# Performance work log

Measured on AMD Instinct MI355X. Metric: run time of the kernel, lower is better.

## Reference

```python
import jax, jax.numpy as jnp
import numpy as np

B, T, K, FT, FP, N, H, HEADS, C = 8, 5, 20, 384, 3, 128, 64, 8, 2
ALPHA = 0.2
NEG = -9e15


def gru(x, Wi, Wh, bi, bh):
    # x: [M, L, F] -> (full [M, L, Hd], last [M, Hd]); torch nn.GRU cell math
    Hd = Wh.shape[0]
    gx = jnp.einsum('mlf,fg->mlg', x, Wi) + bi  # precompute input projections

    def step(h, gxt):
        gh = h @ Wh + bh
        xr, xz, xn = jnp.split(gxt, 3, axis=-1)
        hr, hz, hn = jnp.split(gh, 3, axis=-1)
        r = jax.nn.sigmoid(xr + hr)
        z = jax.nn.sigmoid(xz + hz)
        n = jnp.tanh(xn + r * hn)
        h = (1. - z) * n + z * h
        return h, h

    h0 = jnp.zeros((x.shape[0], Hd), x.dtype)
    last, full = jax.lax.scan(step, h0, jnp.swapaxes(gx, 0, 1))
    return jnp.swapaxes(full, 0, 1), last


def temporal_attn(full, last):
    # attend over time using the last hidden state as the query
    a = jax.nn.softmax(jnp.einsum('mlh,mh->ml', full, last), axis=-1)
    return jnp.einsum('ml,mlh->mh', a, full)


def gat_forward(s, p, adj, sm1_Wi, sm1_Wh, sm1_bi, sm1_bh,
                sm2_Wi, sm2_Wh, sm2_bi, sm2_bh,
                pr_Wi, pr_Wh, pr_bi, pr_bh,
                Wb, bb, Wx, bx, W1, a1, W2, a2):
    mask = adj > 0  # [N, N]
    # --- SMEncoder: vectorized over (batch, stock, day) ---
    s_ = jnp.transpose(s, (0, 4, 1, 2, 3)).reshape(B * N * T, K, FT)
    f1, l1 = gru(s_, sm1_Wi, sm1_Wh, sm1_bi, sm1_bh)
    cv = temporal_attn(f1, l1).reshape(B * N, T, H)          # intra-day context
    f2, l2 = gru(cv, sm2_Wi, sm2_Wh, sm2_bi, sm2_bh)
    ct = temporal_attn(f2, l2).reshape(B, N, H)              # inter-day context
    # --- PriceEncoder: vectorized over (batch, stock) ---
    p_ = jnp.transpose(p, (0, 3, 1, 2)).reshape(B * N, T, FP)
    f3, l3 = gru(p_, pr_Wi, pr_Wh, pr_bi, pr_bh)
    qt = temporal_attn(f3, l3).reshape(B, N, H)
    # --- bilinear fusion + per-stock linear head (dropout is eval-mode identity) ---
    X = jnp.tanh(jnp.einsum('bni,oij,bnj->bno', ct, Wb, qt) + bb)   # [B, N, H]
    out1 = jnp.tanh(jnp.einsum('bnh,nch->bnc', X, Wx) + bx)          # [B, N, C]
    # --- multi-head GAT layer 1 (concat + LeakyReLU + adj-masked softmax) ---
    Whd = jnp.einsum('bnh,khf->bknf', X, W1)                         # [B, heads, N, H]
    e = jax.nn.leaky_relu(
        jnp.einsum('bknf,kf->bkn', Whd, a1[:, :H])[:, :, :, None]
        + jnp.einsum('bknf,kf->bkn', Whd, a1[:, H:])[:, :, None, :], ALPHA)
    att = jax.nn.softmax(jnp.where(mask, e, NEG), axis=-1)
    Xh = jax.nn.elu(jnp.einsum('bknm,bkmf->bknf', att, Whd))
    X2 = jnp.transpose(Xh, (0, 2, 1, 3)).reshape(B, N, HEADS * H)    # head concat
    # --- GAT layer 2 -> num_classes ---
    Wh2 = X2 @ W2                                                    # [B, N, C]
    e2 = jax.nn.leaky_relu((Wh2 @ a2[:C])[:, :, None]
                           + (Wh2 @ a2[C:])[:, None, :], ALPHA)
    att2 = jax.nn.softmax(jnp.where(mask, e2, NEG), axis=-1)
    Xo = jnp.einsum('bnm,bmc->bnc', att2, Wh2)
    return jnp.transpose(Xo + out1, (0, 2, 1))                       # [B, C, N]


def setup_inputs():
    key = jax.random.key(0)
    ks = jax.random.split(key, 23)
    g = lambda k, sh, sc=0.05: jax.random.normal(k, sh, jnp.float32) * sc
    adj = (jax.random.uniform(ks[2], (N, N)) < 0.3).astype(jnp.float32)
    adj = jnp.maximum(adj, jnp.eye(N, dtype=jnp.float32))
    return {
        's': jax.random.normal(ks[0], (B, T, K, FT, N), jnp.float32),
        'p': jax.random.normal(ks[1], (B, T, FP, N), jnp.float32),
        'adj': adj,
        'sm1_Wi': g(ks[3], (FT, 3 * H)), 'sm1_Wh': g(ks[4], (H, 3 * H)),
        'sm1_bi': g(ks[5], (3 * H,)), 'sm1_bh': g(ks[6], (3 * H,)),
        'sm2_Wi': g(ks[7], (H, 3 * H)), 'sm2_Wh': g(ks[8], (H, 3 * H)),
        'sm2_bi': g(ks[9], (3 * H,)), 'sm2_bh': g(ks[10], (3 * H,)),
        'pr_Wi': g(ks[11], (FP, 3 * H)), 'pr_Wh': g(ks[12], (H, 3 * H)),
        'pr_bi': g(ks[13], (3 * H,)), 'pr_bh': g(ks[14], (3 * H,)),
        'Wb': g(ks[15], (H, H, H)), 'bb': g(ks[16], (H,)),
        'Wx': g(ks[17], (N, C, H)), 'bx': g(ks[18], (N, C)),
        'W1': g(ks[19], (HEADS, H, H)), 'a1': g(ks[20], (HEADS, 2 * H)),
        'W2': g(ks[21], (HEADS * H, C)), 'a2': g(ks[22], (2 * C,)),
    }


def reference(s, p, adj, sm1_Wi, sm1_Wh, sm1_bi, sm1_bh,
              sm2_Wi, sm2_Wh, sm2_bi, sm2_bh,
              pr_Wi, pr_Wh, pr_bi, pr_bh,
              Wb, bb, Wx, bx, W1, a1, W2, a2):
    return gat_forward(s, p, adj, sm1_Wi, sm1_Wh, sm1_bi, sm1_bh,
                       sm2_Wi, sm2_Wh, sm2_bi, sm2_bh,
                       pr_Wi, pr_Wh, pr_bi, pr_bh,
                       Wb, bb, Wx, bx, W1, a1, W2, a2)
```

## Files before the change

### kernel.cpp

```cpp
#include <hip/hip_runtime.h>
#include <hip/hip_bf16.h>
#include <hip/hip_fp16.h>

#define DI __device__ __forceinline__

namespace {

constexpr int G_  = 192;
constexpr int FT_ = 384;

typedef _Float16 f16x8 __attribute__((ext_vector_type(8)));
typedef _Float16 f16x4 __attribute__((ext_vector_type(4)));
typedef float    f32x4 __attribute__((ext_vector_type(4)));

DI float lrelu(float x) { return x > 0.f ? x : 0.2f * x; }
DI float sigmoidf(float x) { return 1.f / (1.f + __expf(-x)); }
DI float tanh_fast(float x) { float e = __expf(2.f * x); return 1.f - 2.f / (e + 1.f); }

__global__ __launch_bounds__(256) void k_cvtB(
    const float* __restrict__ Wi, _Float16* __restrict__ Bt) {
  int v = blockIdx.x * 256 + threadIdx.x;
  int g = v / 384, f = v % 384;
  Bt[v] = (_Float16)Wi[f * 192 + g];
}

__global__ __launch_bounds__(256) void k_gx1(
    const float* __restrict__ s, const _Float16* __restrict__ Bt,
    const float* __restrict__ bi, _Float16* __restrict__ gx1) {
  const int slab = blockIdx.x;
  const int b = slab / 100, rem = slab % 100, t = rem / 20, k = rem % 20;
  const float* A = s + (size_t)((b * 5 + t) * 20 + k) * (FT_ * 128);
  __shared__ __align__(16) _Float16 AsL[128 * 40];
  __shared__ __align__(16) _Float16 BsL[192 * 40];
  __shared__ __align__(16) float bisL[192];
  const int tid = threadIdx.x;
  if (tid < 192) bisL[tid] = bi[tid];
  const int w = tid >> 6, l = tid & 63;
  const int lr = l & 15, lk = l >> 4;

  f32x4 acc[12][2];
#pragma unroll
  for (int gt = 0; gt < 12; ++gt)
#pragma unroll
    for (int nt = 0; nt < 2; ++nt) acc[gt][nt] = (f32x4){0.f, 0.f, 0.f, 0.f};

  for (int kc = 0; kc < 12; ++kc) {
    const int f0 = kc * 32;
#pragma unroll
    for (int pass = 0; pass < 2; ++pass) {
      int task = tid + 256 * pass;
      int n = task & 127, oct = task >> 7;
      const float* src = A + (size_t)(f0 + oct * 8) * 128 + n;
      float v[8];
#pragma unroll
      for (int j = 0; j < 8; ++j) v[j] = src[j * 128];
      f16x8 h;
#pragma unroll
      for (int j = 0; j < 8; ++j) h[j] = (_Float16)v[j];
      *(f16x8*)&AsL[n * 40 + oct * 8] = h;
    }
#pragma unroll
    for (int pass = 0; pass < 3; ++pass) {
      int c = tid + 256 * pass;
      int g = c >> 2, oct = c & 3;
      f16x8 h = *(const f16x8*)&Bt[(size_t)g * 384 + f0 + oct * 8];
      *(f16x8*)&BsL[g * 40 + oct * 8] = h;
    }
    __syncthreads();
    f16x8 aN[2];
#pragma unroll
    for (int nt = 0; nt < 2; ++nt)
      aN[nt] = *(const f16x8*)&AsL[(w * 32 + nt * 16 + lr) * 40 + lk * 8];
#pragma unroll
    for (int gt = 0; gt < 12; ++gt) {
      f16x8 bW = *(const f16x8*)&BsL[(gt * 16 + lr) * 40 + lk * 8];
      acc[gt][0] = __builtin_amdgcn_mfma_f32_16x16x32_f16(bW, aN[0], acc[gt][0], 0, 0, 0);
      acc[gt][1] = __builtin_amdgcn_mfma_f32_16x16x32_f16(bW, aN[1], acc[gt][1], 0, 0, 0);
    }
    __syncthreads();
  }
  const size_t base3 = ((size_t)k * 40 + b * 5 + t) * 8;
#pragma unroll
  for (int nt = 0; nt < 2; ++nt) {
    const int ngrp = w * 2 + nt;
    _Float16* dstbase = gx1 + ((base3 + ngrp) * 3) * 1024 + (size_t)l * 16;
#pragma unroll
    for (int gate = 0; gate < 3; ++gate) {
      f16x8 h0, h1;
#pragma unroll
      for (int tq = 0; tq < 4; ++tq) {
        const int gt = gate * 4 + tq;
        f32x4 bias = *(const f32x4*)&bisL[gt * 16 + lk * 4];
        f32x4 c = acc[gt][nt];
#pragma unroll
        for (int r = 0; r < 4; ++r) {
          float v = c[r] + bias[r];
          if (tq < 2) h0[tq * 4 + r] = (_Float16)v;
          else        h1[(tq - 2) * 4 + r] = (_Float16)v;
        }
      }
      *(f16x8*)(dstbase + (size_t)gate * 1024) = h0;
      *(f16x8*)(dstbase + (size_t)gate * 1024 + 8) = h1;
    }
  }
}

__global__ __launch_bounds__(64, 1) void k_scan1m(
    const _Float16* __restrict__ gx, const float* __restrict__ Wh,
    const float* __restrict__ bh, float* __restrict__ cv) {
  const int wv = blockIdx.x;
  const int b = wv / 40, rem = wv % 40, t = rem / 8, ng = rem % 8;
  const int l = threadIdx.x;
  const int seq = l & 15, rg = l >> 4;

  __shared__ __align__(16) _Float16 histL[20][64][24];
  __shared__ __align__(16) _Float16 red[16][72];

  f16x8 whF[12][2];
#pragma unroll
  for (int gt = 0; gt < 12; ++gt)
#pragma unroll
    for (int c = 0; c < 2; ++c) {
      f16x8 h;
#pragma unroll
      for (int j = 0; j < 8; ++j)
        h[j] = (_Float16)Wh[(size_t)(32 * c + rg * 8 + j) * 192 + gt * 16 + seq];
      whF[gt][c] = h;
    }
  f32x4 bhF[12];
#pragma unroll
  for (int gt = 0; gt < 12; ++gt)
    bhF[gt] = *(const f32x4*)&bh[gt * 16 + rg * 4];

  float h16[16];
#pragma unroll
  for (int j = 0; j < 16; ++j) h16[j] = 0.f;

#define GXP(kk) (gx + ((((size_t)(kk) * 40 + b * 5 + t) * 8 + ng) * 3) * 1024 + (size_t)l * 16)

  f16x8 gxc[3][2], gxn[3][2];
  {
    const _Float16* p0 = GXP(0);
    const _Float16* p1 = GXP(1);
#pragma unroll
    for (int g = 0; g < 3; ++g) {
      gxc[g][0] = *(const f16x8*)(p0 + g * 1024);
      gxc[g][1] = *(const f16x8*)(p0 + g * 1024 + 8);
      gxn[g][0] = *(const f16x8*)(p1 + g * 1024);
      gxn[g][1] = *(const f16x8*)(p1 + g * 1024 + 8);
    }
  }

  f16x8 bf0, bf1;
  f32x4 acc[12];

#define GATES_AND_H(KCONST_HIST)                                               \
  {                                                                            \
    _Float16* hp = &histL[KCONST_HIST][l][0];                                  \
    f16x8 p0, p1;                                                              \
    _Pragma("unroll")                                                          \
    for (int tq = 0; tq < 4; ++tq) {                                           \
      _Pragma("unroll")                                                        \
      for (int r = 0; r < 4; ++r) {                                            \
        const int idx = tq * 4 + r;                                            \
        float xr = (float)gxc[0][idx >> 3][idx & 7];                           \
        float xz = (float)gxc[1][idx >> 3][idx & 7];                           \
        float xn = (float)gxc[2][idx >> 3][idx & 7];                           \
        float hr = acc[tq][r], hz = acc[4 + tq][r], hnv = acc[8 + tq][r];      \
        float rr = sigmoidf(xr + hr);                                          \
        float zz = sigmoidf(xz + hz);                                          \
        float nn = tanh_fast(xn + rr * hnv);                                   \
        float hv = (1.f - zz) * nn + zz * h16[idx];                            \
        h16[idx] = hv;                                                         \
        if (idx < 8) p0[idx] = (_Float16)hv; else p1[idx - 8] = (_Float16)hv;  \
      }                                                                        \
    }                                                                          \
    *(f16x8*)hp = p0;                                                          \
    *(f16x8*)(hp + 8) = p1;                                                    \
  }

#define REDIST()                                                               \
  {                                                                            \
    _Pragma("unroll")                                                          \
    for (int tq = 0; tq < 4; ++tq) {                                           \
      f16x4 q;                                                                 \
      q[0] = (_Float16)h16[tq * 4 + 0]; q[1] = (_Float16)h16[tq * 4 + 1];      \
      q[2] = (_Float16)h16[tq * 4 + 2]; q[3] = (_Float16)h16[tq * 4 + 3];      \
      *(f16x4*)&red[seq][16 * tq + 4 * rg] = q;                                \
    }                                                                          \
    bf0 = *(const f16x8*)&red[seq][8 * rg];                                    \
    bf1 = *(const f16x8*)&red[seq][32 + 8 * rg];                               \
  }

#pragma unroll
  for (int gt = 0; gt < 12; ++gt) acc[gt] = bhF[gt];
  GATES_AND_H(0)
  REDIST()

  for (int k = 1; k < 19; ++k) {
#pragma unroll
    for (int g = 0; g < 3; ++g) { gxc[g][0] = gxn[g][0]; gxc[g][1] = gxn[g][1]; }
    const _Float16* pn = GXP(k + 1);
#pragma unroll
    for (int g = 0; g < 3; ++g) {
      gxn[g][0] = *(const f16x8*)(pn + g * 1024);
      gxn[g][1] = *(const f16x8*)(pn + g * 1024 + 8);
    }
#pragma unroll
    for (int gt = 0; gt < 12; ++gt) {
      acc[gt] = bhF[gt];
      acc[gt] = __builtin_amdgcn_mfma_f32_16x16x32_f16(whF[gt][0], bf0, acc[gt], 0, 0, 0);
      acc[gt] = __builtin_amdgcn_mfma_f32_16x16x32_f16(whF[gt][1], bf1, acc[gt], 0, 0, 0);
    }
    GATES_AND_H(k)
    REDIST()
  }

#pragma unroll
  for (int g = 0; g < 3; ++g) { gxc[g][0] = gxn[g][0]; gxc[g][1] = gxn[g][1]; }
#pragma unroll
  for (int gt = 0; gt < 12; ++gt) {
    acc[gt] = bhF[gt];
    acc[gt] = __builtin_amdgcn_mfma_f32_16x16x32_f16(whF[gt][0], bf0, acc[gt], 0, 0, 0);
    acc[gt] = __builtin_amdgcn_mfma_f32_16x16x32_f16(whF[gt][1], bf1, acc[gt], 0, 0, 0);
  }
  GATES_AND_H(19)

  float d[20];
#pragma unroll
  for (int kk = 0; kk < 20; ++kk) {
    f16x8 a0 = *(const f16x8*)&histL[kk][l][0];
    f16x8 a1 = *(const f16x8*)&histL[kk][l][8];
    float p = 0.f;
#pragma unroll
    for (int j = 0; j < 8; ++j)
      p += (float)a0[j] * h16[j] + (float)a1[j] * h16[8 + j];
    p += __shfl_xor(p, 16);
    p += __shfl_xor(p, 32);
    d[kk] = p;
  }
  float mx = d[0];
#pragma unroll
  for (int kk = 1; kk < 20; ++kk) mx = fmaxf(mx, d[kk]);
  float sum = 0.f;
#pragma unroll
  for (int kk = 0; kk < 20; ++kk) { d[kk] = __expf(d[kk] - mx); sum += d[kk]; }
  const float inv = 1.f / sum;
  float av[16];
#pragma unroll
  for (int j = 0; j < 16; ++j) av[j] = 0.f;
#pragma unroll
  for (int kk = 0; kk < 20; ++kk) {
    f16x8 a0 = *(const f16x8*)&histL[kk][l][0];
    f16x8 a1 = *(const f16x8*)&histL[kk][l][8];
    float wgt = d[kk] * inv;
#pragma unroll
    for (int j = 0; j < 8; ++j) {
      av[j]     += wgt * (float)a0[j];
      av[8 + j] += wgt * (float)a1[j];
    }
  }
  const int n = ng * 16 + seq;
  float* dst = cv + ((size_t)(b * 128 + n) * 5 + t) * 64;
#pragma unroll
  for (int tq = 0; tq < 4; ++tq) {
    float4 o = make_float4(av[tq * 4], av[tq * 4 + 1], av[tq * 4 + 2], av[tq * 4 + 3]);
    *(float4*)&dst[16 * tq + 4 * rg] = o;
  }
#undef GXP
#undef GATES_AND_H
#undef REDIST
}

__global__ __launch_bounds__(192) void k_scan2(
    const float* __restrict__ x, const float* __restrict__ Wi,
    const float* __restrict__ Wh, const float* __restrict__ bi,
    const float* __restrict__ bh, float* __restrict__ outv) {
  const int s0 = blockIdx.x * 4;
  const int tid = threadIdx.x;
  __shared__ __align__(16) float hist[4][5][64];
  __shared__ __align__(16) float xl[4][64];
  __shared__ float ghl[4][192], gxl[4][192];
  __shared__ float dls[4][5], als[4][5];
  float wic[64], whc[64];
#pragma unroll
  for (int i = 0; i < 64; ++i) { wic[i] = Wi[i * G_ + tid]; whc[i] = Wh[i * G_ + tid]; }
  const float big = bi[tid], bhg = bh[tid];

  for (int t = 0; t < 5; ++t) {
    for (int v = tid; v < 256; v += 192) {
      int ss = v >> 6, i = v & 63;
      xl[ss][i] = x[((size_t)(s0 + ss) * 5 + t) * 64 + i];
    }
    __syncthreads();
#pragma unroll
    for (int ss = 0; ss < 4; ++ss) {
      const float4* xq = (const float4*)&xl[ss][0];
      float ax = 0.f;
#pragma unroll
      for (int q = 0; q < 16; ++q) {
        float4 v4 = xq[q];
        ax += v4.x * wic[4 * q]     + v4.y * wic[4 * q + 1]
            + v4.z * wic[4 * q + 2] + v4.w * wic[4 * q + 3];
      }
      gxl[ss][tid] = ax + big;
      float ah = 0.f;
      if (t > 0) {
        const float4* hq = (const float4*)&hist[ss][t - 1][0];
#pragma unroll
        for (int q = 0; q < 16; ++q) {
          float4 h4 = hq[q];
          ah += h4.x * whc[4 * q]     + h4.y * whc[4 * q + 1]
              + h4.z * whc[4 * q + 2] + h4.w * whc[4 * q + 3];
        }
      }
      ghl[ss][tid] = ah + bhg;
    }
    __syncthreads();
#pragma unroll
    for (int base = 0; base < 256; base += 192) {
      int tk = base + tid;
      if (tk < 256) {
        int ss = tk >> 6, i = tk & 63;
        float xr = gxl[ss][i], xz = gxl[ss][64 + i], xn = gxl[ss][128 + i];
        float hr = ghl[ss][i], hz = ghl[ss][64 + i], hn = ghl[ss][128 + i];
        float r  = sigmoidf(xr + hr);
        float z  = sigmoidf(xz + hz);
        float nn = tanh_fast(xn + r * hn);
        float hp = (t == 0) ? 0.f : hist[ss][t - 1][i];
        hist[ss][t][i] = (1.f - z) * nn + z * hp;
      }
    }
    __syncthreads();
  }
  if (tid < 20) {
    int ss = tid / 5, kk = tid % 5;
    float d = 0.f;
#pragma unroll
    for (int i = 0; i < 64; ++i) d += hist[ss][kk][i] * hist[ss][4][i];
    dls[ss][kk] = d;
  }
  __syncthreads();
  if (tid < 20) {
    int ss = tid / 5, kk = tid % 5;
    float mx = -3.4e38f;
#pragma unroll
    for (int j = 0; j < 5; ++j) mx = fmaxf(mx, dls[ss][j]);
    als[ss][kk] = __expf(dls[ss][kk] - mx);
  }
  __syncthreads();
  for (int idx = tid; idx < 256; idx += 192) {
    int ss = idx >> 6, i = idx & 63;
    float sum = 0.f, a = 0.f;
#pragma unroll
    for (int kk = 0; kk < 5; ++kk) sum += als[ss][kk];
#pragma unroll
    for (int kk = 0; kk < 5; ++kk) a += als[ss][kk] * hist[ss][kk][i];
    outv[(size_t)(s0 + ss) * 64 + i] = a / sum;
  }
}

__global__ __launch_bounds__(192) void k_scan3(
    const float* __restrict__ p, const float* __restrict__ Wi,
    const float* __restrict__ Wh, const float* __restrict__ bi,
    const float* __restrict__ bh, float* __restrict__ outv) {
  const int s0 = blockIdx.x * 4;
  const int tid = threadIdx.x;
  __shared__ __align__(16) float hist[4][5][64];
  __shared__ float xp[4][3];
  __shared__ float ghl[4][192], gxl[4][192];
  __shared__ float dls[4][5], als[4][5];
  float wic[3], whc[64];
#pragma unroll
  for (int f = 0; f < 3; ++f) wic[f] = Wi[f * G_ + tid];
#pragma unroll
  for (int i = 0; i < 64; ++i) whc[i] = Wh[i * G_ + tid];
  const float big = bi[tid], bhg = bh[tid];

  for (int t = 0; t < 5; ++t) {
    if (tid < 12) {
      int ss = tid / 3, f = tid % 3;
      int seq = s0 + ss, b = seq >> 7, n = seq & 127;
      xp[ss][f] = p[((size_t)(b * 5 + t) * 3 + f) * 128 + n];
    }
    __syncthreads();
#pragma unroll
    for (int ss = 0; ss < 4; ++ss) {
      gxl[ss][tid] = xp[ss][0] * wic[0] + xp[ss][1] * wic[1] + xp[ss][2] * wic[2] + big;
      float ah = 0.f;
      if (t > 0) {
        const float4* hq = (const float4*)&hist[ss][t - 1][0];
#pragma unroll
        for (int q = 0; q < 16; ++q) {
          float4 h4 = hq[q];
          ah += h4.x * whc[4 * q]     + h4.y * whc[4 * q + 1]
              + h4.z * whc[4 * q + 2] + h4.w * whc[4 * q + 3];
        }
      }
      ghl[ss][tid] = ah + bhg;
    }
    __syncthreads();
#pragma unroll
    for (int base = 0; base < 256; base += 192) {
      int tk = base + tid;
      if (tk < 256) {
        int ss = tk >> 6, i = tk & 63;
        float xr = gxl[ss][i], xz = gxl[ss][64 + i], xn = gxl[ss][128 + i];
        float hr = ghl[ss][i], hz = ghl[ss][64 + i], hn = ghl[ss][128 + i];
        float r  = sigmoidf(xr + hr);
        float z  = sigmoidf(xz + hz);
        float nn = tanh_fast(xn + r * hn);
        float hp = (t == 0) ? 0.f : hist[ss][t - 1][i];
        hist[ss][t][i] = (1.f - z) * nn + z * hp;
      }
    }
    __syncthreads();
  }
  if (tid < 20) {
    int ss = tid / 5, kk = tid % 5;
    float d = 0.f;
#pragma unroll
    for (int i = 0; i < 64; ++i) d += hist[ss][kk][i] * hist[ss][4][i];
    dls[ss][kk] = d;
  }
  __syncthreads();
  if (tid < 20) {
    int ss = tid / 5, kk = tid % 5;
    float mx = -3.4e38f;
#pragma unroll
    for (int j = 0; j < 5; ++j) mx = fmaxf(mx, dls[ss][j]);
    als[ss][kk] = __expf(dls[ss][kk] - mx);
  }
  __syncthreads();
  for (int idx = tid; idx < 256; idx += 192) {
    int ss = idx >> 6, i = idx & 63;
    float sum = 0.f, a = 0.f;
#pragma unroll
    for (int kk = 0; kk < 5; ++kk) sum += als[ss][kk];
#pragma unroll
    for (int kk = 0; kk < 5; ++kk) a += als[ss][kk] * hist[ss][kk][i];
    outv[(size_t)(s0 + ss) * 64 + i] = a / sum;
  }
}

__global__ __launch_bounds__(256) void k_bilinear(
    const float* __restrict__ ct, const float* __restrict__ qt,
    const float* __restrict__ Wb, const float* __restrict__ bb,
    float* __restrict__ X) {
  const int bn0 = blockIdx.x * 4;
  const int tid = threadIdx.x;
  __shared__ float ctl[4][64], qtl[4][64];
  {
    int ss = tid >> 6, i = tid & 63;
    ctl[ss][i] = ct[(size_t)(bn0 + ss) * 64 + i];
    qtl[ss][i] = qt[(size_t)(bn0 + ss) * 64 + i];
  }
  __syncthreads();
  const int o = tid >> 2, part = tid & 3, j0 = part << 4;
  float qr[4][16];
#pragma unroll
  for (int pp = 0; pp < 4; ++pp)
#pragma unroll
    for (int q = 0; q < 16; ++q) qr[pp][q] = qtl[pp][j0 + q];
  float acc[4] = {0.f, 0.f, 0.f, 0.f};
  const float* wb = Wb + (size_t)o * 4096 + j0;
  for (int i = 0; i < 64; ++i) {
    const float4* w4 = (const float4*)(wb + i * 64);
    float tmp[4] = {0.f, 0.f, 0.f, 0.f};
#pragma unroll
    for (int q = 0; q < 4; ++q) {
      float4 w = w4[q];
#pragma unroll
      for (int pp = 0; pp < 4; ++pp)
        tmp[pp] += w.x * qr[pp][4 * q]     + w.y * qr[pp][4 * q + 1]
                 + w.z * qr[pp][4 * q + 2] + w.w * qr[pp][4 * q + 3];
    }
#pragma unroll
    for (int pp = 0; pp < 4; ++pp) acc[pp] += ctl[pp][i] * tmp[pp];
  }
#pragma unroll
  for (int pp = 0; pp < 4; ++pp) {
    acc[pp] += __shfl_xor(acc[pp], 1);
    acc[pp] += __shfl_xor(acc[pp], 2);
  }
  if (part == 0) {
    float bbv = bb[o];
#pragma unroll
    for (int pp = 0; pp < 4; ++pp)
      X[(size_t)(bn0 + pp) * 64 + o] = tanh_fast(acc[pp] + bbv);
  }
}

__global__ __launch_bounds__(256) void k_gat1(
    const float* __restrict__ X, const float* __restrict__ W1,
    const float* __restrict__ a1, const float* __restrict__ adj,
    float* __restrict__ X2) {
  const int b = blockIdx.x >> 3, k = blockIdx.x & 7;
  const int tid = threadIdx.x;
  __shared__ __align__(16) float whd[128][68];
  __shared__ float w1l[64][64];
  __shared__ float d1l[128], d2l[128];
  for (int v = tid; v < 4096; v += 256) w1l[v >> 6][v & 63] = W1[(size_t)k * 4096 + v];
  __syncthreads();
  {
    const int f = tid & 63, ng = tid >> 6;
    const float* Xb = X + (size_t)b * 128 * 64;
    for (int n = ng * 32; n < ng * 32 + 32; ++n) {
      float a = 0.f;
#pragma unroll
      for (int h = 0; h < 64; ++h) a += Xb[n * 64 + h] * w1l[h][f];
      whd[n][f] = a;
    }
  }
  __syncthreads();
  if (tid < 128) {
    const int n = tid;
    float da = 0.f, db = 0.f;
#pragma unroll
    for (int f = 0; f < 64; ++f) {
      float w = whd[n][f];
      da += w * a1[k * 128 + f];
      db += w * a1[k * 128 + 64 + f];
    }
    d1l[n] = da; d2l[n] = db;
  }
  __syncthreads();
  {
    const int n = tid & 127, fh = tid >> 7;
    unsigned long long mlo = 0ull, mhi = 0ull;
    for (int m = 0; m < 64; ++m) if (adj[n * 128 + m] > 0.f)      mlo |= (1ull << m);
    for (int m = 0; m < 64; ++m) if (adj[n * 128 + 64 + m] > 0.f) mhi |= (1ull << m);
    const float d1n = d1l[n];
    float mx = -3.4e38f;
    for (int m = 0; m < 128; ++m) {
      bool on = (m < 64) ? (((mlo >> m) & 1ull) != 0) : (((mhi >> (m - 64)) & 1ull) != 0);
      float e = lrelu(d1n + d2l[m]);
      mx = fmaxf(mx, on ? e : -3.4e38f);
    }
    float sum = 0.f;
    float acc[32];
#pragma unroll
    for (int q = 0; q < 32; ++q) acc[q] = 0.f;
    for (int m = 0; m < 128; ++m) {
      bool on = (m < 64) ? (((mlo >> m) & 1ull) != 0) : (((mhi >> (m - 64)) & 1ull) != 0);
      float w = on ? __expf(lrelu(d1n + d2l[m]) - mx) : 0.f;
      sum += w;
      const float4* wr = (const float4*)&whd[m][fh * 32];
#pragma unroll
      for (int q8 = 0; q8 < 8; ++q8) {
        float4 wv = wr[q8];
        acc[4 * q8]     += w * wv.x;
        acc[4 * q8 + 1] += w * wv.y;
        acc[4 * q8 + 2] += w * wv.z;
        acc[4 * q8 + 3] += w * wv.w;
      }
    }
    float inv = 1.f / sum;
    float* dst = X2 + ((size_t)b * 128 + n) * 512 + k * 64 + fh * 32;
#pragma unroll
    for (int q = 0; q < 32; ++q) {
      float v = acc[q] * inv;
      dst[q] = v > 0.f ? v : (__expf(v) - 1.f);
    }
  }
}

__global__ __launch_bounds__(256) void k_head(
    const float* __restrict__ X, const float* __restrict__ Wx, const float* __restrict__ bx,
    const float* __restrict__ X2, const float* __restrict__ W2, const float* __restrict__ a2,
    const float* __restrict__ adj, float* __restrict__ out) {
  const int b = blockIdx.x;
  const int tid = threadIdx.x;
  __shared__ float w2l[1024];
  __shared__ float wh2l[128][2];
  __shared__ float d2aL[128], d2bL[128];
  __shared__ float out1L[128][2];
  for (int v = tid; v < 1024; v += 256) w2l[v] = W2[v];
  __syncthreads();
  const int w = tid >> 6, l = tid & 63;
  const float a20 = a2[0], a21 = a2[1], a22 = a2[2], a23 = a2[3];
  for (int it = 0; it < 32; ++it) {
    int n = w * 32 + it;
    const float* xr = X2 + ((size_t)b * 128 + n) * 512 + l * 8;
    float4 xa = *(const float4*)xr;
    float4 xb = *(const float4*)(xr + 4);
    float xs[8] = {xa.x, xa.y, xa.z, xa.w, xb.x, xb.y, xb.z, xb.w};
    float s0 = 0.f, s1 = 0.f;
#pragma unroll
    for (int j = 0; j < 8; ++j) {
      s0 += xs[j] * w2l[(l * 8 + j) * 2];
      s1 += xs[j] * w2l[(l * 8 + j) * 2 + 1];
    }
#pragma unroll
    for (int d = 1; d < 64; d <<= 1) { s0 += __shfl_xor(s0, d); s1 += __shfl_xor(s1, d); }
    if (l == 0) {
      wh2l[n][0] = s0; wh2l[n][1] = s1;
      d2aL[n] = s0 * a20 + s1 * a21;
      d2bL[n] = s0 * a22 + s1 * a23;
    }
  }
  if (tid < 128) {
    int n = tid;
    const float* xrow = X + ((size_t)b * 128 + n) * 64;
#pragma unroll
    for (int c = 0; c < 2; ++c) {
      float a = 0.f;
#pragma unroll
      for (int h = 0; h < 64; ++h) a += xrow[h] * Wx[(n * 2 + c) * 64 + h];
      out1L[n][c] = tanh_fast(a + bx[n * 2 + c]);
    }
  }
  __syncthreads();
  if (tid < 128) {
    const int n = tid;
    unsigned long long mlo = 0ull, mhi = 0ull;
    for (int m = 0; m < 64; ++m) if (adj[n * 128 + m] > 0.f)      mlo |= (1ull << m);
    for (int m = 0; m < 64; ++m) if (adj[n * 128 + 64 + m] > 0.f) mhi |= (1ull << m);
    const float dan = d2aL[n];
    float mx = -3.4e38f;
    for (int m = 0; m < 128; ++m) {
      bool on = (m < 64) ? (((mlo >> m) & 1ull) != 0) : (((mhi >> (m - 64)) & 1ull) != 0);
      float e = lrelu(dan + d2bL[m]);
      mx = fmaxf(mx, on ? e : -3.4e38f);
    }
    float sum = 0.f, x0 = 0.f, x1 = 0.f;
    for (int m = 0; m < 128; ++m) {
      bool on = (m < 64) ? (((mlo >> m) & 1ull) != 0) : (((mhi >> (m - 64)) & 1ull) != 0);
      float wgt = on ? __expf(lrelu(dan + d2bL[m]) - mx) : 0.f;
      sum += wgt; x0 += wgt * wh2l[m][0]; x1 += wgt * wh2l[m][1];
    }
    float inv = 1.f / sum;
    out[(size_t)(b * 2 + 0) * 128 + n] = x0 * inv + out1L[n][0];
    out[(size_t)(b * 2 + 1) * 128 + n] = x1 * inv + out1L[n][1];
  }
}

}

extern "C" void kernel_launch(void* const* d_in, const int* in_sizes, int n_in,
                              void* d_out, int out_size, void* d_ws, size_t ws_size,
                              hipStream_t stream) {
  (void)in_sizes; (void)n_in; (void)out_size;
  const float* s      = (const float*)d_in[0];
  const float* p      = (const float*)d_in[1];
  const float* adj    = (const float*)d_in[2];
  const float* sm1_Wi = (const float*)d_in[3];
  const float* sm1_Wh = (const float*)d_in[4];
  const float* sm1_bi = (const float*)d_in[5];
  const float* sm1_bh = (const float*)d_in[6];
  const float* sm2_Wi = (const float*)d_in[7];
  const float* sm2_Wh = (const float*)d_in[8];
  const float* sm2_bi = (const float*)d_in[9];
  const float* sm2_bh = (const float*)d_in[10];
  const float* pr_Wi  = (const float*)d_in[11];
  const float* pr_Wh  = (const float*)d_in[12];
  const float* pr_bi  = (const float*)d_in[13];
  const float* pr_bh  = (const float*)d_in[14];
  const float* Wb     = (const float*)d_in[15];
  const float* bb     = (const float*)d_in[16];
  const float* Wx     = (const float*)d_in[17];
  const float* bx     = (const float*)d_in[18];
  const float* W1     = (const float*)d_in[19];
  const float* a1     = (const float*)d_in[20];
  const float* W2     = (const float*)d_in[21];
  const float* a2     = (const float*)d_in[22];

  if (ws_size < 43515904u) return;
  char* ws = (char*)d_ws;
  _Float16* gx1 = (_Float16*)ws;
  float* cv   = (float*)(ws + 39321600);
  float* ct   = (float*)(ws + 40632320);
  float* qt   = (float*)(ws + 40894464);
  float* X    = (float*)(ws + 41156608);
  float* X2   = (float*)(ws + 41418752);
  _Float16* Bt = (_Float16*)(ws + 41418752);

  hipLaunchKernelGGL(k_cvtB,     dim3(288),  dim3(256), 0, stream, sm1_Wi, Bt);
  hipLaunchKernelGGL(k_gx1,      dim3(800),  dim3(256), 0, stream, s, Bt, sm1_bi, gx1);
  hipLaunchKernelGGL(k_scan1m,   dim3(320),  dim3(64),  0, stream, gx1, sm1_Wh, sm1_bh, cv);
  hipLaunchKernelGGL(k_scan2,    dim3(256),  dim3(192), 0, stream, cv, sm2_Wi, sm2_Wh, sm2_bi, sm2_bh, ct);
  hipLaunchKernelGGL(k_scan3,    dim3(256),  dim3(192), 0, stream, p, pr_Wi, pr_Wh, pr_bi, pr_bh, qt);
  hipLaunchKernelGGL(k_bilinear, dim3(256),  dim3(256), 0, stream, ct, qt, Wb, bb, X);
  hipLaunchKernelGGL(k_gat1,     dim3(64),   dim3(256), 0, stream, X, W1, a1, adj, X2);
  hipLaunchKernelGGL(k_head,     dim3(8),    dim3(256), 0, stream, X, Wx, bx, X2, W2, a2, adj, (float*)d_out);
}
```

Before: 503.3 us.

## Rewrite scan2 with MFMA, deepen gx prefetch, split GAT head kernels

Replaces the scalar scan2 GRU with an MFMA-based single-wave kernel that reads fp16 intra-day contexts written by scan1. scan1 now prefetches gx two steps ahead instead of one. gat1 gets twice as many blocks and the head kernel is split into a wider wh2/out1 kernel plus a small final softmax kernel, which adds one launch. Divides are replaced with hardware reciprocal, and the fp16 intermediate plus approximate rcp add a small precision cost.

Result: faster. 476.5 us (-5.3%).

```diff
diff --git a/kernel.cpp b/kernel.cpp
--- a/kernel.cpp
+++ b/kernel.cpp
@@ -13,9 +13,10 @@
 typedef _Float16 f16x4 __attribute__((ext_vector_type(4)));
 typedef float    f32x4 __attribute__((ext_vector_type(4)));
 
+DI float rcpf(float x) { return __builtin_amdgcn_rcpf(x); }
 DI float lrelu(float x) { return x > 0.f ? x : 0.2f * x; }
-DI float sigmoidf(float x) { return 1.f / (1.f + __expf(-x)); }
-DI float tanh_fast(float x) { float e = __expf(2.f * x); return 1.f - 2.f / (e + 1.f); }
+DI float sigmoidf(float x) { return rcpf(1.f + __expf(-x)); }
+DI float tanh_fast(float x) { return 1.f - 2.f * rcpf(__expf(2.f * x) + 1.f); }
 
 __global__ __launch_bounds__(256) void k_cvtB(
     const float* __restrict__ Wi, _Float16* __restrict__ Bt) {
@@ -107,7 +108,7 @@
 
 __global__ __launch_bounds__(64, 1) void k_scan1m(
     const _Float16* __restrict__ gx, const float* __restrict__ Wh,
-    const float* __restrict__ bh, float* __restrict__ cv) {
+    const float* __restrict__ bh, _Float16* __restrict__ cvh) {
   const int wv = blockIdx.x;
   const int b = wv / 40, rem = wv % 40, t = rem / 8, ng = rem % 8;
   const int l = threadIdx.x;
@@ -138,16 +139,19 @@
 
 #define GXP(kk) (gx + ((((size_t)(kk) * 40 + b * 5 + t) * 8 + ng) * 3) * 1024 + (size_t)l * 16)
 
-  f16x8 gxc[3][2], gxn[3][2];
+  f16x8 gxc[3][2], gxn[3][2], gxn2[3][2];
   {
     const _Float16* p0 = GXP(0);
     const _Float16* p1 = GXP(1);
+    const _Float16* p2 = GXP(2);
 #pragma unroll
     for (int g = 0; g < 3; ++g) {
-      gxc[g][0] = *(const f16x8*)(p0 + g * 1024);
-      gxc[g][1] = *(const f16x8*)(p0 + g * 1024 + 8);
-      gxn[g][0] = *(const f16x8*)(p1 + g * 1024);
-      gxn[g][1] = *(const f16x8*)(p1 + g * 1024 + 8);
+      gxc[g][0]  = *(const f16x8*)(p0 + g * 1024);
+      gxc[g][1]  = *(const f16x8*)(p0 + g * 1024 + 8);
+      gxn[g][0]  = *(const f16x8*)(p1 + g * 1024);
+      gxn[g][1]  = *(const f16x8*)(p1 + g * 1024 + 8);
+      gxn2[g][0] = *(const f16x8*)(p2 + g * 1024);
+      gxn2[g][1] = *(const f16x8*)(p2 + g * 1024 + 8);
     }
   }
 
@@ -199,12 +203,17 @@
 
   for (int k = 1; k < 19; ++k) {
 #pragma unroll
-    for (int g = 0; g < 3; ++g) { gxc[g][0] = gxn[g][0]; gxc[g][1] = gxn[g][1]; }
-    const _Float16* pn = GXP(k + 1);
-#pragma unroll
     for (int g = 0; g < 3; ++g) {
-      gxn[g][0] = *(const f16x8*)(pn + g * 1024);
-      gxn[g][1] = *(const f16x8*)(pn + g * 1024 + 8);
+      gxc[g][0] = gxn[g][0];  gxc[g][1] = gxn[g][1];
+      gxn[g][0] = gxn2[g][0]; gxn[g][1] = gxn2[g][1];
+    }
+    if (k < 18) {
+      const _Float16* pn = GXP(k + 2);
+#pragma unroll
+      for (int g = 0; g < 3; ++g) {
+        gxn2[g][0] = *(const f16x8*)(pn + g * 1024);
+        gxn2[g][1] = *(const f16x8*)(pn + g * 1024 + 8);
+      }
     }
 #pragma unroll
     for (int gt = 0; gt < 12; ++gt) {
@@ -245,7 +254,7 @@
   float sum = 0.f;
 #pragma unroll
   for (int kk = 0; kk < 20; ++kk) { d[kk] = __expf(d[kk] - mx); sum += d[kk]; }
-  const float inv = 1.f / sum;
+  const float inv = rcpf(sum);
   float av[16];
 #pragma unroll
   for (int j = 0; j < 16; ++j) av[j] = 0.f;
@@ -261,49 +270,174 @@
     }
   }
   const int n = ng * 16 + seq;
-  float* dst = cv + ((size_t)(b * 128 + n) * 5 + t) * 64;
+  const size_t seqg = (size_t)b * 128 + n;
+  _Float16* dst = cvh + (seqg * 5 + t) * 64;
+#pragma unroll
+  for (int tq = 0; tq < 4; ++tq) {
+    f16x4 q;
+    q[0] = (_Float16)av[tq * 4 + 0]; q[1] = (_Float16)av[tq * 4 + 1];
+    q[2] = (_Float16)av[tq * 4 + 2]; q[3] = (_Float16)av[tq * 4 + 3];
+    *(f16x4*)&dst[16 * tq + 4 * rg] = q;
+  }
+#undef GXP
+#undef GATES_AND_H
+#undef REDIST
+}
+
+__global__ __launch_bounds__(64, 1) void k_scan2m(
+    const _Float16* __restrict__ cvh, const float* __restrict__ Wi,
+    const float* __restrict__ Wh, const float* __restrict__ bi,
+    const float* __restrict__ bh, float* __restrict__ ct) {
+  const int l = threadIdx.x;
+  const int seq = l & 15, rg = l >> 4;
+  const size_t seqg0 = (size_t)blockIdx.x * 16;
+
+  __shared__ __align__(16) _Float16 histL[5][64][24];
+  __shared__ __align__(16) _Float16 red[16][72];
+
+  f16x8 wiF[12][2], whF[12][2];
+#pragma unroll
+  for (int gt = 0; gt < 12; ++gt)
+#pragma unroll
+    for (int c = 0; c < 2; ++c) {
+      f16x8 hi, hh;
+#pragma unroll
+      for (int j = 0; j < 8; ++j) {
+        hi[j] = (_Float16)Wi[(size_t)(32 * c + rg * 8 + j) * 192 + gt * 16 + seq];
+        hh[j] = (_Float16)Wh[(size_t)(32 * c + rg * 8 + j) * 192 + gt * 16 + seq];
+      }
+      wiF[gt][c] = hi; whF[gt][c] = hh;
+    }
+  f32x4 biF[12], bhF[12];
+#pragma unroll
+  for (int gt = 0; gt < 12; ++gt) {
+    biF[gt] = *(const f32x4*)&bi[gt * 16 + rg * 4];
+    bhF[gt] = *(const f32x4*)&bh[gt * 16 + rg * 4];
+  }
+
+  float h16[16];
+#pragma unroll
+  for (int j = 0; j < 16; ++j) h16[j] = 0.f;
+  f16x8 bf0, bf1;
+
+#pragma unroll
+  for (int t = 0; t < 5; ++t) {
+    const _Float16* xp = cvh + ((seqg0 + seq) * 5 + t) * 64;
+    f16x8 xf0 = *(const f16x8*)(xp + 8 * rg);
+    f16x8 xf1 = *(const f16x8*)(xp + 32 + 8 * rg);
+    f32x4 accX[12], accH[12];
+#pragma unroll
+    for (int gt = 0; gt < 12; ++gt) {
+      accX[gt] = biF[gt];
+      accX[gt] = __builtin_amdgcn_mfma_f32_16x16x32_f16(wiF[gt][0], xf0, accX[gt], 0, 0, 0);
+      accX[gt] = __builtin_amdgcn_mfma_f32_16x16x32_f16(wiF[gt][1], xf1, accX[gt], 0, 0, 0);
+      accH[gt] = bhF[gt];
+      if (t > 0) {
+        accH[gt] = __builtin_amdgcn_mfma_f32_16x16x32_f16(whF[gt][0], bf0, accH[gt], 0, 0, 0);
+        accH[gt] = __builtin_amdgcn_mfma_f32_16x16x32_f16(whF[gt][1], bf1, accH[gt], 0, 0, 0);
+      }
+    }
+    _Float16* hp = &histL[t][l][0];
+    f16x8 p0, p1;
+#pragma unroll
+    for (int tq = 0; tq < 4; ++tq) {
+#pragma unroll
+      for (int r = 0; r < 4; ++r) {
+        const int idx = tq * 4 + r;
+        float xr = accX[tq][r], xz = accX[4 + tq][r], xn = accX[8 + tq][r];
+        float hr = accH[tq][r], hz = accH[4 + tq][r], hnv = accH[8 + tq][r];
+        float rr = sigmoidf(xr + hr);
+        float zz = sigmoidf(xz + hz);
+        float nn = tanh_fast(xn + rr * hnv);
+        float hv = (1.f - zz) * nn + zz * h16[idx];
+        h16[idx] = hv;
+        if (idx < 8) p0[idx] = (_Float16)hv; else p1[idx - 8] = (_Float16)hv;
+      }
+    }
+    *(f16x8*)hp = p0;
+    *(f16x8*)(hp + 8) = p1;
+    if (t < 4) {
+#pragma unroll
+      for (int tq = 0; tq < 4; ++tq) {
+        f16x4 q;
+        q[0] = (_Float16)h16[tq * 4 + 0]; q[1] = (_Float16)h16[tq * 4 + 1];
+        q[2] = (_Float16)h16[tq * 4 + 2]; q[3] = (_Float16)h16[tq * 4 + 3];
+        *(f16x4*)&red[seq][16 * tq + 4 * rg] = q;
+      }
+      bf0 = *(const f16x8*)&red[seq][8 * rg];
+      bf1 = *(const f16x8*)&red[seq][32 + 8 * rg];
+    }
+  }
+
+  float d[5];
+#pragma unroll
+  for (int kk = 0; kk < 5; ++kk) {
+    f16x8 a0 = *(const f16x8*)&histL[kk][l][0];
+    f16x8 a1 = *(const f16x8*)&histL[kk][l][8];
+    float p = 0.f;
+#pragma unroll
+    for (int j = 0; j < 8; ++j)
+      p += (float)a0[j] * h16[j] + (float)a1[j] * h16[8 + j];
+    p += __shfl_xor(p, 16);
+    p += __shfl_xor(p, 32);
+    d[kk] = p;
+  }
+  float mx = d[0];
+#pragma unroll
+  for (int kk = 1; kk < 5; ++kk) mx = fmaxf(mx, d[kk]);
+  float sum = 0.f;
+#pragma unroll
+  for (int kk = 0; kk < 5; ++kk) { d[kk] = __expf(d[kk] - mx); sum += d[kk]; }
+  const float inv = rcpf(sum);
+  float av[16];
+#pragma unroll
+  for (int j = 0; j < 16; ++j) av[j] = 0.f;
+#pragma unroll
+  for (int kk = 0; kk < 5; ++kk) {
+    f16x8 a0 = *(const f16x8*)&histL[kk][l][0];
+    f16x8 a1 = *(const f16x8*)&histL[kk][l][8];
+    float wgt = d[kk] * inv;
+#pragma unroll
+    for (int j = 0; j < 8; ++j) {
+      av[j]     += wgt * (float)a0[j];
+      av[8 + j] += wgt * (float)a1[j];
+    }
+  }
+  float* dst = ct + (seqg0 + seq) * 64;
 #pragma unroll
   for (int tq = 0; tq < 4; ++tq) {
     float4 o = make_float4(av[tq * 4], av[tq * 4 + 1], av[tq * 4 + 2], av[tq * 4 + 3]);
     *(float4*)&dst[16 * tq + 4 * rg] = o;
   }
-#undef GXP
-#undef GATES_AND_H
-#undef REDIST
-}
-
-__global__ __launch_bounds__(192) void k_scan2(
-    const float* __restrict__ x, const float* __restrict__ Wi,
+}
+
+__global__ __launch_bounds__(192) void k_scan3(
+    const float* __restrict__ p, const float* __restrict__ Wi,
     const float* __restrict__ Wh, const float* __restrict__ bi,
     const float* __restrict__ bh, float* __restrict__ outv) {
   const int s0 = blockIdx.x * 4;
   const int tid = threadIdx.x;
   __shared__ __align__(16) float hist[4][5][64];
-  __shared__ __align__(16) float xl[4][64];
+  __shared__ float xp[4][3];
   __shared__ float ghl[4][192], gxl[4][192];
   __shared__ float dls[4][5], als[4][5];
-  float wic[64], whc[64];
-#pragma unroll
-  for (int i = 0; i < 64; ++i) { wic[i] = Wi[i * G_ + tid]; whc[i] = Wh[i * G_ + tid]; }
+  float wic[3], whc[64];
+#pragma unroll
+  for (int f = 0; f < 3; ++f) wic[f] = Wi[f * G_ + tid];
+#pragma unroll
+  for (int i = 0; i < 64; ++i) whc[i] = Wh[i * G_ + tid];
   const float big = bi[tid], bhg = bh[tid];
 
   for (int t = 0; t < 5; ++t) {
-    for (int v = tid; v < 256; v += 192) {
-      int ss = v >> 6, i = v & 63;
-      xl[ss][i] = x[((size_t)(s0 + ss) * 5 + t) * 64 + i];
+    if (tid < 12) {
+      int ss = tid / 3, f = tid % 3;
+      int seq = s0 + ss, b = seq >> 7, n = seq & 127;
+      xp[ss][f] = p[((size_t)(b * 5 + t) * 3 + f) * 128 + n];
     }
     __syncthreads();
 #pragma unroll
     for (int ss = 0; ss < 4; ++ss) {
-      const float4* xq = (const float4*)&xl[ss][0];
-      float ax = 0.f;
-#pragma unroll
-      for (int q = 0; q < 16; ++q) {
-        float4 v4 = xq[q];
-        ax += v4.x * wic[4 * q]     + v4.y * wic[4 * q + 1]
-            + v4.z * wic[4 * q + 2] + v4.w * wic[4 * q + 3];
-      }
-      gxl[ss][tid] = ax + big;
+      gxl[ss][tid] = xp[ss][0] * wic[0] + xp[ss][1] * wic[1] + xp[ss][2] * wic[2] + big;
       float ah = 0.f;
       if (t > 0) {
         const float4* hq = (const float4*)&hist[ss][t - 1][0];
@@ -356,90 +490,7 @@
     for (int kk = 0; kk < 5; ++kk) sum += als[ss][kk];
 #pragma unroll
     for (int kk = 0; kk < 5; ++kk) a += als[ss][kk] * hist[ss][kk][i];
-    outv[(size_t)(s0 + ss) * 64 + i] = a / sum;
-  }
-}
-
-__global__ __launch_bounds__(192) void k_scan3(
-    const float* __restrict__ p, const float* __restrict__ Wi,
-    const float* __restrict__ Wh, const float* __restrict__ bi,
-    const float* __restrict__ bh, float* __restrict__ outv) {
-  const int s0 = blockIdx.x * 4;
-  const int tid = threadIdx.x;
-  __shared__ __align__(16) float hist[4][5][64];
-  __shared__ float xp[4][3];
-  __shared__ float ghl[4][192], gxl[4][192];
-  __shared__ float dls[4][5], als[4][5];
-  float wic[3], whc[64];
-#pragma unroll
-  for (int f = 0; f < 3; ++f) wic[f] = Wi[f * G_ + tid];
-#pragma unroll
-  for (int i = 0; i < 64; ++i) whc[i] = Wh[i * G_ + tid];
-  const float big = bi[tid], bhg = bh[tid];
-
-  for (int t = 0; t < 5; ++t) {
-    if (tid < 12) {
-      int ss = tid / 3, f = tid % 3;
-      int seq = s0 + ss, b = seq >> 7, n = seq & 127;
-      xp[ss][f] = p[((size_t)(b * 5 + t) * 3 + f) * 128 + n];
-    }
-    __syncthreads();
-#pragma unroll
-    for (int ss = 0; ss < 4; ++ss) {
-      gxl[ss][tid] = xp[ss][0] * wic[0] + xp[ss][1] * wic[1] + xp[ss][2] * wic[2] + big;
-      float ah = 0.f;
-      if (t > 0) {
-        const float4* hq = (const float4*)&hist[ss][t - 1][0];
-#pragma unroll
-        for (int q = 0; q < 16; ++q) {
-          float4 h4 = hq[q];
-          ah += h4.x * whc[4 * q]     + h4.y * whc[4 * q + 1]
-              + h4.z * whc[4 * q + 2] + h4.w * whc[4 * q + 3];
-        }
-      }
-      ghl[ss][tid] = ah + bhg;
-    }
-    __syncthreads();
-#pragma unroll
-    for (int base = 0; base < 256; base += 192) {
-      int tk = base + tid;
-      if (tk < 256) {
-        int ss = tk >> 6, i = tk & 63;
-        float xr = gxl[ss][i], xz = gxl[ss][64 + i], xn = gxl[ss][128 + i];
-        float hr = ghl[ss][i], hz = ghl[ss][64 + i], hn = ghl[ss][128 + i];
-        float r  = sigmoidf(xr + hr);
-        float z  = sigmoidf(xz + hz);
-        float nn = tanh_fast(xn + r * hn);
-        float hp = (t == 0) ? 0.f : hist[ss][t - 1][i];
-        hist[ss][t][i] = (1.f - z) * nn + z * hp;
-      }
-    }
-    __syncthreads();
-  }
-  if (tid < 20) {
-    int ss = tid / 5, kk = tid % 5;
-    float d = 0.f;
-#pragma unroll
-    for (int i = 0; i < 64; ++i) d += hist[ss][kk][i] * hist[ss][4][i];
-    dls[ss][kk] = d;
-  }
-  __syncthreads();
-  if (tid < 20) {
-    int ss = tid / 5, kk = tid % 5;
-    float mx = -3.4e38f;
-#pragma unroll
-    for (int j = 0; j < 5; ++j) mx = fmaxf(mx, dls[ss][j]);
-    als[ss][kk] = __expf(dls[ss][kk] - mx);
-  }
-  __syncthreads();
-  for (int idx = tid; idx < 256; idx += 192) {
-    int ss = idx >> 6, i = idx & 63;
-    float sum = 0.f, a = 0.f;
-#pragma unroll
-    for (int kk = 0; kk < 5; ++kk) sum += als[ss][kk];
-#pragma unroll
-    for (int kk = 0; kk < 5; ++kk) a += als[ss][kk] * hist[ss][kk][i];
-    outv[(size_t)(s0 + ss) * 64 + i] = a / sum;
+    outv[(size_t)(s0 + ss) * 64 + i] = a * rcpf(sum);
   }
 }
 
@@ -495,7 +546,8 @@
     const float* __restrict__ X, const float* __restrict__ W1,
     const float* __restrict__ a1, const float* __restrict__ adj,
     float* __restrict__ X2) {
-  const int b = blockIdx.x >> 3, k = blockIdx.x & 7;
+  const int bid = blockIdx.x;
+  const int b = bid >> 4, k = (bid >> 1) & 7, nh = bid & 1;
   const int tid = threadIdx.x;
   __shared__ __align__(16) float whd[128][68];
   __shared__ float w1l[64][64];
@@ -526,7 +578,7 @@
   }
   __syncthreads();
   {
-    const int n = tid & 127, fh = tid >> 7;
+    const int n = nh * 64 + (tid & 63), fq = tid >> 6, f0 = fq * 16;
     unsigned long long mlo = 0ull, mhi = 0ull;
     for (int m = 0; m < 64; ++m) if (adj[n * 128 + m] > 0.f)      mlo |= (1ull << m);
     for (int m = 0; m < 64; ++m) if (adj[n * 128 + 64 + m] > 0.f) mhi |= (1ull << m);
@@ -538,50 +590,50 @@
       mx = fmaxf(mx, on ? e : -3.4e38f);
     }
     float sum = 0.f;
-    float acc[32];
-#pragma unroll
-    for (int q = 0; q < 32; ++q) acc[q] = 0.f;
+    float acc[16];
+#pragma unroll
+    for (int q = 0; q < 16; ++q) acc[q] = 0.f;
     for (int m = 0; m < 128; ++m) {
       bool on = (m < 64) ? (((mlo >> m) & 1ull) != 0) : (((mhi >> (m - 64)) & 1ull) != 0);
       float w = on ? __expf(lrelu(d1n + d2l[m]) - mx) : 0.f;
       sum += w;
-      const float4* wr = (const float4*)&whd[m][fh * 32];
-#pragma unroll
-      for (int q8 = 0; q8 < 8; ++q8) {
-        float4 wv = wr[q8];
-        acc[4 * q8]     += w * wv.x;
-        acc[4 * q8 + 1] += w * wv.y;
-        acc[4 * q8 + 2] += w * wv.z;
-        acc[4 * q8 + 3] += w * wv.w;
-      }
-    }
-    float inv = 1.f / sum;
-    float* dst = X2 + ((size_t)b * 128 + n) * 512 + k * 64 + fh * 32;
-#pragma unroll
-    for (int q = 0; q < 32; ++q) {
+      const float4* wr = (const float4*)&whd[m][f0];
+#pragma unroll
+      for (int q4 = 0; q4 < 4; ++q4) {
+        float4 wv = wr[q4];
+        acc[4 * q4]     += w * wv.x;
+        acc[4 * q4 + 1] += w * wv.y;
+        acc[4 * q4 + 2] += w * wv.z;
+        acc[4 * q4 + 3] += w * wv.w;
+      }
+    }
+    float inv = rcpf(sum);
+    float* dst = X2 + ((size_t)b * 128 + n) * 512 + k * 64 + f0;
+#pragma unroll
+    for (int q = 0; q < 16; ++q) {
       float v = acc[q] * inv;
       dst[q] = v > 0.f ? v : (__expf(v) - 1.f);
     }
   }
 }
 
-__global__ __launch_bounds__(256) void k_head(
+__global__ __launch_bounds__(256) void k_wh2(
     const float* __restrict__ X, const float* __restrict__ Wx, const float* __restrict__ bx,
     const float* __restrict__ X2, const float* __restrict__ W2, const float* __restrict__ a2,
-    const float* __restrict__ adj, float* __restrict__ out) {
-  const int b = blockIdx.x;
+    float* __restrict__ out1g, float* __restrict__ wh2g,
+    float* __restrict__ d2ag, float* __restrict__ d2bg) {
+  const int b = blockIdx.x >> 3, nq = blockIdx.x & 7;
   const int tid = threadIdx.x;
   __shared__ float w2l[1024];
-  __shared__ float wh2l[128][2];
-  __shared__ float d2aL[128], d2bL[128];
-  __shared__ float out1L[128][2];
   for (int v = tid; v < 1024; v += 256) w2l[v] = W2[v];
   __syncthreads();
   const int w = tid >> 6, l = tid & 63;
   const float a20 = a2[0], a21 = a2[1], a22 = a2[2], a23 = a2[3];
-  for (int it = 0; it < 32; ++it) {
-    int n = w * 32 + it;
-    const float* xr = X2 + ((size_t)b * 128 + n) * 512 + l * 8;
+#pragma unroll
+  for (int it = 0; it < 4; ++it) {
+    int n = nq * 16 + w * 4 + it;
+    int bn = b * 128 + n;
+    const float* xr = X2 + (size_t)bn * 512 + l * 8;
     float4 xa = *(const float4*)xr;
     float4 xb = *(const float4*)(xr + 4);
     float xs[8] = {xa.x, xa.y, xa.z, xa.w, xb.x, xb.y, xb.z, xb.w};
@@ -594,45 +646,54 @@
 #pragma unroll
     for (int d = 1; d < 64; d <<= 1) { s0 += __shfl_xor(s0, d); s1 += __shfl_xor(s1, d); }
     if (l == 0) {
-      wh2l[n][0] = s0; wh2l[n][1] = s1;
-      d2aL[n] = s0 * a20 + s1 * a21;
-      d2bL[n] = s0 * a22 + s1 * a23;
-    }
-  }
-  if (tid < 128) {
-    int n = tid;
-    const float* xrow = X + ((size_t)b * 128 + n) * 64;
-#pragma unroll
-    for (int c = 0; c < 2; ++c) {
-      float a = 0.f;
-#pragma unroll
-      for (int h = 0; h < 64; ++h) a += xrow[h] * Wx[(n * 2 + c) * 64 + h];
-      out1L[n][c] = tanh_fast(a + bx[n * 2 + c]);
-    }
-  }
+      wh2g[bn * 2] = s0; wh2g[bn * 2 + 1] = s1;
+      d2ag[bn] = s0 * a20 + s1 * a21;
+      d2bg[bn] = s0 * a22 + s1 * a23;
+    }
+  }
+  if (tid < 32) {
+    int n = nq * 16 + (tid >> 1), c = tid & 1;
+    int bn = b * 128 + n;
+    const float* xrow = X + (size_t)bn * 64;
+    float a = 0.f;
+#pragma unroll
+    for (int h = 0; h < 64; ++h) a += xrow[h] * Wx[(n * 2 + c) * 64 + h];
+    out1g[bn * 2 + c] = tanh_fast(a + bx[n * 2 + c]);
+  }
+}
+
+__global__ __launch_bounds__(128) void k_final(
+    const float* __restrict__ adj, const float* __restrict__ wh2g,
+    const float* __restrict__ d2ag, const float* __restrict__ d2bg,
+    const float* __restrict__ out1g, float* __restrict__ out) {
+  const int b = blockIdx.x;
+  const int tid = threadIdx.x;
+  __shared__ float wh2l[128][2];
+  __shared__ float dbl_[128];
+  wh2l[tid][0] = wh2g[(size_t)(b * 128 + tid) * 2];
+  wh2l[tid][1] = wh2g[(size_t)(b * 128 + tid) * 2 + 1];
+  dbl_[tid] = d2bg[b * 128 + tid];
   __syncthreads();
-  if (tid < 128) {
-    const int n = tid;
-    unsigned long long mlo = 0ull, mhi = 0ull;
-    for (int m = 0; m < 64; ++m) if (adj[n * 128 + m] > 0.f)      mlo |= (1ull << m);
-    for (int m = 0; m < 64; ++m) if (adj[n * 128 + 64 + m] > 0.f) mhi |= (1ull << m);
-    const float dan = d2aL[n];
-    float mx = -3.4e38f;
-    for (int m = 0; m < 128; ++m) {
-      bool on = (m < 64) ? (((mlo >> m) & 1ull) != 0) : (((mhi >> (m - 64)) & 1ull) != 0);
-      float e = lrelu(dan + d2bL[m]);
-      mx = fmaxf(mx, on ? e : -3.4e38f);
-    }
-    float sum = 0.f, x0 = 0.f, x1 = 0.f;
-    for (int m = 0; m < 128; ++m) {
-      bool on = (m < 64) ? (((mlo >> m) & 1ull) != 0) : (((mhi >> (m - 64)) & 1ull) != 0);
-      float wgt = on ? __expf(lrelu(dan + d2bL[m]) - mx) : 0.f;
-      sum += wgt; x0 += wgt * wh2l[m][0]; x1 += wgt * wh2l[m][1];
-    }
-    float inv = 1.f / sum;
-    out[(size_t)(b * 2 + 0) * 128 + n] = x0 * inv + out1L[n][0];
-    out[(size_t)(b * 2 + 1) * 128 + n] = x1 * inv + out1L[n][1];
-  }
+  const int n = tid;
+  unsigned long long mlo = 0ull, mhi = 0ull;
+  for (int m = 0; m < 64; ++m) if (adj[n * 128 + m] > 0.f)      mlo |= (1ull << m);
+  for (int m = 0; m < 64; ++m) if (adj[n * 128 + 64 + m] > 0.f) mhi |= (1ull << m);
+  const float dan = d2ag[b * 128 + n];
+  float mx = -3.4e38f;
+  for (int m = 0; m < 128; ++m) {
+    bool on = (m < 64) ? (((mlo >> m) & 1ull) != 0) : (((mhi >> (m - 64)) & 1ull) != 0);
+    float e = lrelu(dan + dbl_[m]);
+    mx = fmaxf(mx, on ? e : -3.4e38f);
+  }
+  float sum = 0.f, x0 = 0.f, x1 = 0.f;
+  for (int m = 0; m < 128; ++m) {
+    bool on = (m < 64) ? (((mlo >> m) & 1ull) != 0) : (((mhi >> (m - 64)) & 1ull) != 0);
+    float w = on ? __expf(lrelu(dan + dbl_[m]) - mx) : 0.f;
+    sum += w; x0 += w * wh2l[m][0]; x1 += w * wh2l[m][1];
+  }
+  float inv = rcpf(sum);
+  out[(size_t)(b * 2 + 0) * 128 + n] = x0 * inv + out1g[(size_t)(b * 128 + n) * 2];
+  out[(size_t)(b * 2 + 1) * 128 + n] = x1 * inv + out1g[(size_t)(b * 128 + n) * 2 + 1];
 }
 
 }
@@ -665,22 +726,27 @@
   const float* W2     = (const float*)d_in[21];
   const float* a2     = (const float*)d_in[22];
 
-  if (ws_size < 43515904u) return;
+  if (ws_size < 43540480u) return;
   char* ws = (char*)d_ws;
-  _Float16* gx1 = (_Float16*)ws;
-  float* cv   = (float*)(ws + 39321600);
-  float* ct   = (float*)(ws + 40632320);
-  float* qt   = (float*)(ws + 40894464);
-  float* X    = (float*)(ws + 41156608);
-  float* X2   = (float*)(ws + 41418752);
-  _Float16* Bt = (_Float16*)(ws + 41418752);
+  _Float16* gx1  = (_Float16*)ws;
+  _Float16* cvh  = (_Float16*)(ws + 39321600);
+  float* ct      = (float*)(ws + 40632320);
+  float* qt      = (float*)(ws + 40894464);
+  float* X       = (float*)(ws + 41156608);
+  float* X2      = (float*)(ws + 41418752);
+  _Float16* Bt   = (_Float16*)(ws + 41418752);
+  float* wh2g    = (float*)(ws + 43515904);
+  float* out1g   = (float*)(ws + 43524096);
+  float* d2ag    = (float*)(ws + 43532288);
+  float* d2bg    = (float*)(ws + 43536384);
 
   hipLaunchKernelGGL(k_cvtB,     dim3(288),  dim3(256), 0, stream, sm1_Wi, Bt);
   hipLaunchKernelGGL(k_gx1,      dim3(800),  dim3(256), 0, stream, s, Bt, sm1_bi, gx1);
-  hipLaunchKernelGGL(k_scan1m,   dim3(320),  dim3(64),  0, stream, gx1, sm1_Wh, sm1_bh, cv);
-  hipLaunchKernelGGL(k_scan2,    dim3(256),  dim3(192), 0, stream, cv, sm2_Wi, sm2_Wh, sm2_bi, sm2_bh, ct);
+  hipLaunchKernelGGL(k_scan1m,   dim3(320),  dim3(64),  0, stream, gx1, sm1_Wh, sm1_bh, cvh);
+  hipLaunchKernelGGL(k_scan2m,   dim3(64),   dim3(64),  0, stream, cvh, sm2_Wi, sm2_Wh, sm2_bi, sm2_bh, ct);
   hipLaunchKernelGGL(k_scan3,    dim3(256),  dim3(192), 0, stream, p, pr_Wi, pr_Wh, pr_bi, pr_bh, qt);
   hipLaunchKernelGGL(k_bilinear, dim3(256),  dim3(256), 0, stream, ct, qt, Wb, bb, X);
-  hipLaunchKernelGGL(k_gat1,     dim3(64),   dim3(256), 0, stream, X, W1, a1, adj, X2);
-  hipLaunchKernelGGL(k_head,     dim3(8),    dim3(256), 0, stream, X, Wx, bx, X2, W2, a2, adj, (float*)d_out);
-}
+  hipLaunchKernelGGL(k_gat1,     dim3(128),  dim3(256), 0, stream, X, W1, a1, adj, X2);
+  hipLaunchKernelGGL(k_wh2,      dim3(64),   dim3(256), 0, stream, X, Wx, bx, X2, W2, a2, out1g, wh2g, d2ag, d2bg);
+  hipLaunchKernelGGL(k_final,    dim3(8),    dim3(128), 0, stream, adj, wh2g, d2ag, d2bg, out1g, (float*)d_out);
+}
```
